# Kernel optimization log

Measured on AMD Instinct MI355X. Metric: run time of the kernel, lower is better.

Reference implementation:

```python
import jax, jax.numpy as jnp
import numpy as np

B, N, D = 2, 2048, 2048
H = 16
HD = D // H          # 128
R = 512              # kv_rank
INT4_MIN, INT4_MAX = -8, 7


def setup_inputs() -> dict:
    key = jax.random.key(0)
    ks = jax.random.split(key, 6)
    sD = 1.0 / np.sqrt(D)
    sR = 1.0 / np.sqrt(R)
    return {
        "x":   jax.random.normal(ks[0], (B, N, D), dtype=jnp.float32),
        "Wq":  jax.random.normal(ks[1], (D, D), dtype=jnp.float32) * sD,
        "bq":  jnp.zeros((D,), dtype=jnp.float32),
        "Wkv": jax.random.normal(ks[2], (D, R), dtype=jnp.float32) * sD,
        "bkv": jnp.zeros((R,), dtype=jnp.float32),
        "Wku": jax.random.normal(ks[3], (R, D), dtype=jnp.float32) * sR,
        "bku": jnp.zeros((D,), dtype=jnp.float32),
        "Wvu": jax.random.normal(ks[4], (R, D), dtype=jnp.float32) * sR,
        "bvu": jnp.zeros((D,), dtype=jnp.float32),
        "Wo":  jax.random.normal(ks[5], (D, D), dtype=jnp.float32) * sD * 0.1,
        "bo":  jnp.zeros((D,), dtype=jnp.float32),
    }


def _int4_quant_dequant(t):
    # per_channel=True, 3D tensor: amax over dims [0,1], keepdim
    amax = jnp.max(jnp.abs(t), axis=(0, 1), keepdims=True)
    amax = jnp.maximum(amax, 1e-5)
    scale = (amax / 7.0).astype(jnp.float32)
    q = jnp.clip(jnp.round(t / scale), INT4_MIN, INT4_MAX).astype(jnp.int8)
    return q.astype(jnp.float32) * scale


def reference(x, Wq, bq, Wkv, bkv, Wku, bku, Wvu, bvu, Wo, bo):
    q = x @ Wq + bq                              # (B,N,D)
    kv_latent = x @ Wkv + bkv                    # (B,N,R)
    kv_latent = _int4_quant_dequant(kv_latent)   # use_cache=True path
    k = kv_latent @ Wku + bku                    # (B,N,D)
    v = kv_latent @ Wvu + bvu                    # (B,N,D)

    q4 = q.reshape(B, N, H, HD)
    k4 = k.reshape(B, N, H, HD)
    v4 = v.reshape(B, N, H, HD)

    attn = jnp.einsum("bqhd,bkhd->bhqk", q4, k4) * (HD ** -0.5)
    attn = jax.nn.softmax(attn.astype(jnp.float32), axis=-1).astype(x.dtype)
    out = jnp.einsum("bhqk,bkhd->bqhd", attn, v4).reshape(B, N, D)
    return out @ Wo + bo
```

## Files before the change

### kernel.cpp

```cpp
#include <hip/hip_runtime.h>
#include <stdint.h>

typedef __attribute__((ext_vector_type(8))) _Float16 half8;
typedef __attribute__((ext_vector_type(4))) _Float16 half4;
typedef __attribute__((ext_vector_type(2))) __fp16 fp16x2;
typedef __attribute__((ext_vector_type(4))) float f32x4;

#define AS1 __attribute__((address_space(1)))
#define AS3 __attribute__((address_space(3)))

__device__ inline void gload_lds16(const void* g, void* l) {
  __builtin_amdgcn_global_load_lds((const AS1 void*)g, (AS3 void*)l, 16, 0, 0);
}
__device__ inline f32x4 mfma16h(half8 a, half8 b, f32x4 c) {
  return __builtin_amdgcn_mfma_f32_16x16x32_f16(a, b, c, 0, 0, 0);
}

__global__ __launch_bounds__(256) void cvt_split(const float4* __restrict__ in,
                                                 half4* __restrict__ xh,
                                                 half4* __restrict__ xl, int nq) {
  int i = blockIdx.x * 256 + threadIdx.x;
  if (i >= nq) return;
  float4 v = in[i];
  float vv[4] = {v.x, v.y, v.z, v.w};
  half4 h, lo;
#pragma unroll
  for (int j = 0; j < 4; ++j) {
    _Float16 hh = (_Float16)vv[j];
    h[j] = hh;
    lo[j] = (_Float16)((vv[j] - (float)hh) * 4096.0f);
  }
  xh[i] = h;
  xl[i] = lo;
}

__global__ __launch_bounds__(256) void transpose_f16(const float* __restrict__ in,
                                                     const float* __restrict__ in2,
                                                     _Float16* __restrict__ outh,
                                                     _Float16* __restrict__ outl,
                                                     const float* __restrict__ rowamax,
                                                     int R, int C) {
  __shared__ float t[32][33];
  if (blockIdx.z) { in = in2; outh += (size_t)R * C; }
  const int tx = threadIdx.x, ty = threadIdx.y;
  const int r0 = blockIdx.y * 32, c0 = blockIdx.x * 32;
#pragma unroll
  for (int k = 0; k < 4; ++k) {
    const int r = r0 + ty + k * 8;
    float s = 1.0f;
    if (rowamax) s = fmaxf(rowamax[r], 1e-5f) / 7.0f;
    t[ty + k * 8][tx] = in[(size_t)r * C + c0 + tx] * s;
  }
  __syncthreads();
#pragma unroll
  for (int k = 0; k < 4; ++k) {
    const int c = c0 + ty + k * 8;
    float v = t[tx][ty + k * 8];
    _Float16 h = (_Float16)v;
    outh[(size_t)c * R + r0 + tx] = h;
    if (outl) outl[(size_t)c * R + r0 + tx] = (_Float16)((v - (float)h) * 4096.0f);
  }
}

__global__ __launch_bounds__(256) void gemm_kv16(const _Float16* __restrict__ Ah,
                                                 const _Float16* __restrict__ Al,
                                                 const _Float16* __restrict__ Bh,
                                                 const _Float16* __restrict__ Bl,
                                                 const float* __restrict__ bias,
                                                 float* __restrict__ C,
                                                 float* __restrict__ amax,
                                                 int M, int N, int K) {
  __shared__ _Float16 sAh[64 * 64], sAl[64 * 64];
  __shared__ _Float16 sBh[64 * 64], sBl[64 * 64];
  const int tid = threadIdx.x;
  const int w = tid >> 6, l = tid & 63, g = l >> 4, c = l & 15;
  const int wr = w >> 1, wc = w & 1;
  int wgid = blockIdx.x + blockIdx.y * gridDim.x;
  const int nwg = gridDim.x * gridDim.y;
  wgid = (wgid & 7) * (nwg >> 3) + (wgid >> 3);
  const int tm0 = (wgid / gridDim.x) * 64, n0 = (wgid % gridDim.x) * 64;

  f32x4 acc[2][2], acc2[2][2];
#pragma unroll
  for (int i = 0; i < 2; ++i)
#pragma unroll
    for (int j = 0; j < 2; ++j) {
      acc[i][j] = f32x4{0.f, 0.f, 0.f, 0.f};
      acc2[i][j] = f32x4{0.f, 0.f, 0.f, 0.f};
    }

  for (int k0 = 0; k0 < K; k0 += 64) {
#pragma unroll
    for (int cc = 0; cc < 2; ++cc) {
      const int off = w * 2048 + cc * 1024 + l * 16;
      const int row = off >> 7, colb = off & 127;
      const char* gA = (const char*)Ah + ((size_t)(tm0 + row) * K + k0) * 2 + colb;
      const char* gL = (const char*)Al + ((size_t)(tm0 + row) * K + k0) * 2 + colb;
      gload_lds16(gA, (char*)sAh + w * 2048 + cc * 1024);
      gload_lds16(gL, (char*)sAl + w * 2048 + cc * 1024);
    }
#pragma unroll
    for (int cc = 0; cc < 2; ++cc) {
      const int off = w * 2048 + cc * 1024 + l * 16;
      const int row = off >> 7, colb = off & 127;
      const char* gB = (const char*)Bh + ((size_t)(n0 + row) * K + k0) * 2 + colb;
      const char* gL = (const char*)Bl + ((size_t)(n0 + row) * K + k0) * 2 + colb;
      gload_lds16(gB, (char*)sBh + w * 2048 + cc * 1024);
      gload_lds16(gL, (char*)sBl + w * 2048 + cc * 1024);
    }
    __syncthreads();
#pragma unroll
    for (int ks = 0; ks < 2; ++ks) {
      half8 ah[2], al[2], bh[2], bl[2];
#pragma unroll
      for (int i = 0; i < 2; ++i) {
        ah[i] = *(const half8*)&sAh[(wr * 32 + i * 16 + c) * 64 + ks * 32 + g * 8];
        al[i] = *(const half8*)&sAl[(wr * 32 + i * 16 + c) * 64 + ks * 32 + g * 8];
      }
#pragma unroll
      for (int j = 0; j < 2; ++j) {
        bh[j] = *(const half8*)&sBh[(wc * 32 + j * 16 + c) * 64 + ks * 32 + g * 8];
        bl[j] = *(const half8*)&sBl[(wc * 32 + j * 16 + c) * 64 + ks * 32 + g * 8];
      }
#pragma unroll
      for (int i = 0; i < 2; ++i)
#pragma unroll
        for (int j = 0; j < 2; ++j) {
          acc[i][j] = mfma16h(ah[i], bh[j], acc[i][j]);
          acc2[i][j] = mfma16h(al[i], bh[j], acc2[i][j]);
          acc2[i][j] = mfma16h(ah[i], bl[j], acc2[i][j]);
        }
    }
    __syncthreads();
  }

  float cm[2] = {0.f, 0.f};
#pragma unroll
  for (int i = 0; i < 2; ++i) {
    const int row0 = tm0 + wr * 32 + i * 16 + g * 4;
#pragma unroll
    for (int j = 0; j < 2; ++j) {
      const int col = n0 + wc * 32 + j * 16 + c;
      const float bv = bias[col];
#pragma unroll
      for (int r = 0; r < 4; ++r) {
        float v = acc[i][j][r] + acc2[i][j][r] * 2.44140625e-4f + bv;
        C[(size_t)(row0 + r) * N + col] = v;
        cm[j] = fmaxf(cm[j], fabsf(v));
      }
    }
  }
#pragma unroll
  for (int j = 0; j < 2; ++j) {
    float m = cm[j];
    m = fmaxf(m, __shfl_xor(m, 16, 64));
    m = fmaxf(m, __shfl_xor(m, 32, 64));
    if (g == 0) atomicMax((int*)amax + (n0 + wc * 32 + j * 16 + c), __float_as_int(m));
  }
}

__global__ __launch_bounds__(256) void quant_kernel(const float4* __restrict__ kv,
                                                    const float* __restrict__ amax,
                                                    half4* __restrict__ kvq, int nq) {
  int i = blockIdx.x * 256 + threadIdx.x;
  if (i >= nq) return;
  float4 v = kv[i];
  int r0 = (i * 4) & 511;
  half4 o;
#pragma unroll
  for (int j = 0; j < 4; ++j) {
    float s = fmaxf(amax[r0 + j], 1e-5f) / 7.0f;
    float val = (j == 0) ? v.x : (j == 1) ? v.y : (j == 2) ? v.z : v.w;
    float q = rintf(val / s);
    q = fminf(7.f, fmaxf(-8.f, q));
    o[j] = (_Float16)q;
  }
  kvq[i] = o;
}

template <int MODE>
__global__ __launch_bounds__(256) void gemm_bt(const _Float16* __restrict__ A,
                                               const _Float16* __restrict__ BT,
                                               void* __restrict__ Cout,
                                               void* __restrict__ Cout2,
                                               const float* __restrict__ bias,
                                               const float* __restrict__ bias2,
                                               float cscale,
                                               int M, int N, int K) {
  __shared__ _Float16 As[128 * 64];
  __shared__ _Float16 Bs[128 * 64];
  const int tid = threadIdx.x;
  const int w = tid >> 6, l = tid & 63, g = l >> 4, c = l & 15;
  const int wr = w >> 1, wc = w & 1;
  int wgid = blockIdx.x + blockIdx.y * gridDim.x;
  const int nwg = gridDim.x * gridDim.y;
  wgid = (wgid & 7) * (nwg >> 3) + (wgid >> 3);
  const int tm0 = (wgid / gridDim.x) * 128, tn0 = (wgid % gridDim.x) * 128;

  f32x4 acc[4][4];
#pragma unroll
  for (int i = 0; i < 4; ++i)
#pragma unroll
    for (int j = 0; j < 4; ++j) acc[i][j] = f32x4{0.f, 0.f, 0.f, 0.f};

  for (int k0 = 0; k0 < K; k0 += 64) {
#pragma unroll
    for (int cc = 0; cc < 4; ++cc) {
      const int off = w * 4096 + cc * 1024 + l * 16;
      const int row = off >> 7, colb = off & 127;
      const char* gA = (const char*)A + ((size_t)(tm0 + row) * K + k0) * 2 + colb;
      const char* gB = (const char*)BT + ((size_t)(tn0 + row) * K + k0) * 2 + colb;
      gload_lds16(gA, (char*)As + w * 4096 + cc * 1024);
      gload_lds16(gB, (char*)Bs + w * 4096 + cc * 1024);
    }
    __syncthreads();
#pragma unroll
    for (int ks = 0; ks < 2; ++ks) {
      half8 a[4], b[4];
#pragma unroll
      for (int i = 0; i < 4; ++i)
        a[i] = *(const half8*)&As[(wr * 64 + i * 16 + c) * 64 + ks * 32 + g * 8];
#pragma unroll
      for (int j = 0; j < 4; ++j)
        b[j] = *(const half8*)&Bs[(wc * 64 + j * 16 + c) * 64 + ks * 32 + g * 8];
#pragma unroll
      for (int i = 0; i < 4; ++i)
#pragma unroll
        for (int j = 0; j < 4; ++j) acc[i][j] = mfma16h(a[i], b[j], acc[i][j]);
    }
    __syncthreads();
  }

#pragma unroll
  for (int i = 0; i < 4; ++i) {
    const int row0 = tm0 + wr * 64 + i * 16 + g * 4;
#pragma unroll
    for (int j = 0; j < 4; ++j) {
      const int col = tn0 + wc * 64 + j * 16 + c;
      if constexpr (MODE == 0) {
        const float bv = bias[col];
#pragma unroll
        for (int r = 0; r < 4; ++r)
          ((_Float16*)Cout)[(size_t)(row0 + r) * N + col] =
              (_Float16)((acc[i][j][r] + bv) * cscale);
      } else if constexpr (MODE == 4) {
        const int bI = row0 >> 11;
        const int colk = col & 2047;
        const int hI = colk >> 7, dI = colk & 127;
        if (col < 2048) {
          const float bv = bias[colk];
#pragma unroll
          for (int r = 0; r < 4; ++r) {
            const int n = (row0 + r) & 2047;
            ((_Float16*)Cout)[(size_t)((bI * 16 + hI) * 32 + (n >> 6)) * 8192 +
                              (n & 63) * 128 + dI] = (_Float16)(acc[i][j][r] + bv);
          }
        } else {
          const float bv = bias2[colk];
          half4 pk;
#pragma unroll
          for (int r = 0; r < 4; ++r) pk[r] = (_Float16)(acc[i][j][r] + bv);
          const int nI = row0 & 2047;
          *(half4*)((_Float16*)Cout2 +
                    (size_t)((bI * 16 + hI) * 32 + (nI >> 6)) * 8192 + dI * 64 + (nI & 63)) = pk;
        }
      } else {
        const float bv = bias[col];
#pragma unroll
        for (int r = 0; r < 4; ++r)
          ((float*)Cout)[(size_t)(row0 + r) * N + col] = acc[i][j][r] + bv;
      }
    }
  }
}

__global__ __launch_bounds__(256, 2) void flash_attn(const _Float16* __restrict__ Q,
                                                     const _Float16* __restrict__ KB,
                                                     const _Float16* __restrict__ VB,
                                                     _Float16* __restrict__ O) {
  __shared__ _Float16 Ks[2][8192];
  __shared__ _Float16 Vs[2][8192];
  __shared__ _Float16 Ps[4][2048];
  const int tid = threadIdx.x, w = tid >> 6, l = tid & 63, g = l >> 4, c = l & 15;
  const int wgid = blockIdx.x + blockIdx.y * 16;
  const int xcd = wgid & 7, idx = wgid >> 3;
  const int bh = xcd * 4 + (idx >> 4), qblk = idx & 15;
  const int b = bh >> 4, h = bh & 15;
  const size_t rowQ0 = (size_t)b * 2048 + qblk * 128 + w * 32;
  const _Float16* kvK = KB + (size_t)bh * 262144;
  const _Float16* kvV = VB + (size_t)bh * 262144;
  const int sw = (c & 7) << 4;

  auto stageK = [&](int t, int buf) {
#pragma unroll
    for (int i = 0; i < 4; ++i) {
      const int o = i * 4096 + w * 1024 + l * 16;
      const int row = o >> 8;
      const int src = (o & ~255) | ((o & 255) ^ ((row & 7) << 4));
      gload_lds16((const char*)(kvK + t * 8192) + src,
                  (char*)&Ks[buf][0] + i * 4096 + w * 1024);
    }
  };
  auto stageV = [&](int t, int buf) {
#pragma unroll
    for (int i = 0; i < 4; ++i) {
      const int o = i * 4096 + w * 1024 + l * 16;
      const int row = o >> 7;
      const int src = (o & ~127) | ((o & 127) ^ ((row & 7) << 4));
      gload_lds16((const char*)(kvV + t * 8192) + src,
                  (char*)&Vs[buf][0] + i * 4096 + w * 1024);
    }
  };

  stageK(0, 0);
  stageV(0, 0);
  half8 bq[2][4];
#pragma unroll
  for (int m = 0; m < 2; ++m)
#pragma unroll
    for (int ks = 0; ks < 4; ++ks)
      bq[m][ks] = *(const half8*)&Q[(rowQ0 + m * 16 + c) * 2048 + h * 128 + ks * 32 + g * 8];

  f32x4 accO[2][8];
#pragma unroll
  for (int m = 0; m < 2; ++m)
#pragma unroll
    for (int n = 0; n < 8; ++n) accO[m][n] = f32x4{0.f, 0.f, 0.f, 0.f};
  float lsum[2] = {0.f, 0.f};

  __syncthreads();

  for (int t = 0; t < 32; ++t) {
    const int cur = t & 1;
    if (t < 31) { stageK(t + 1, cur ^ 1); stageV(t + 1, cur ^ 1); }
    f32x4 accS[2][4];
#pragma unroll
    for (int m = 0; m < 2; ++m)
#pragma unroll
      for (int n = 0; n < 4; ++n) accS[m][n] = f32x4{0.f, 0.f, 0.f, 0.f};
    __builtin_amdgcn_s_setprio(1);
#pragma unroll
    for (int ks = 0; ks < 4; ++ks) {
      half8 ak[4];
#pragma unroll
      for (int n = 0; n < 4; ++n) {
        const int row = n * 16 + c;
        ak[n] = *(const half8*)((const char*)&Ks[cur][0] + row * 256 +
                                ((ks * 64 + g * 16) ^ sw));
      }
#pragma unroll
      for (int m = 0; m < 2; ++m)
#pragma unroll
        for (int n = 0; n < 4; ++n) accS[m][n] = mfma16h(ak[n], bq[m][ks], accS[m][n]);
    }
    __builtin_amdgcn_s_setprio(0);
#pragma unroll
    for (int m = 0; m < 2; ++m)
#pragma unroll
      for (int n = 0; n < 4; ++n) {
        const float p0 = exp2f(accS[m][n][0]);
        const float p1 = exp2f(accS[m][n][1]);
        const float p2 = exp2f(accS[m][n][2]);
        const float p3 = exp2f(accS[m][n][3]);
        lsum[m] += (p0 + p1) + (p2 + p3);
        fp16x2 lo = __builtin_amdgcn_cvt_pkrtz(p0, p1);
        fp16x2 hi = __builtin_amdgcn_cvt_pkrtz(p2, p3);
        uint2 u;
        u.x = __builtin_bit_cast(unsigned, lo);
        u.y = __builtin_bit_cast(unsigned, hi);
        *(uint2*)((char*)&Ps[w][0] + (m * 16 + c) * 128 +
                  ((n * 32 + g * 8) ^ sw)) = u;
      }
    __builtin_amdgcn_s_setprio(1);
#pragma unroll
    for (int ks = 0; ks < 2; ++ks) {
      half8 bp[2];
#pragma unroll
      for (int m = 0; m < 2; ++m)
        bp[m] = *(const half8*)((const char*)&Ps[w][0] + (m * 16 + c) * 128 +
                                ((ks * 64 + g * 16) ^ sw));
#pragma unroll
      for (int n = 0; n < 8; ++n) {
        half8 av = *(const half8*)((const char*)&Vs[cur][0] + (n * 16 + c) * 128 +
                                   ((ks * 64 + g * 16) ^ sw));
#pragma unroll
        for (int m = 0; m < 2; ++m) accO[m][n] = mfma16h(av, bp[m], accO[m][n]);
      }
    }
    __builtin_amdgcn_s_setprio(0);
    __syncthreads();
  }

#pragma unroll
  for (int m = 0; m < 2; ++m) {
    float ps = lsum[m];
    ps += __shfl_xor(ps, 16, 64);
    ps += __shfl_xor(ps, 32, 64);
    const float inv = 1.f / ps;
    const size_t qrow = rowQ0 + m * 16 + c;
#pragma unroll
    for (int n = 0; n < 8; ++n) {
      half4 pk;
#pragma unroll
      for (int r = 0; r < 4; ++r) pk[r] = (_Float16)(accO[m][n][r] * inv);
      *(half4*)&O[qrow * 2048 + h * 128 + n * 16 + g * 4] = pk;
    }
  }
}

#define SCALE_QK 0.08838834764831845f
#define LOG2E    1.4426950408889634f

extern "C" void kernel_launch(void* const* d_in, const int* in_sizes, int n_in,
                              void* d_out, int out_size, void* d_ws, size_t ws_size,
                              hipStream_t stream) {
  const float* x   = (const float*)d_in[0];
  const float* Wq  = (const float*)d_in[1];
  const float* bq  = (const float*)d_in[2];
  const float* Wkv = (const float*)d_in[3];
  const float* bkv = (const float*)d_in[4];
  const float* Wku = (const float*)d_in[5];
  const float* bku = (const float*)d_in[6];
  const float* Wvu = (const float*)d_in[7];
  const float* bvu = (const float*)d_in[8];
  const float* Wo  = (const float*)d_in[9];
  const float* bo  = (const float*)d_in[10];
  float* out = (float*)d_out;

  char* ws = (char*)d_ws;
  const size_t MB = 1ull << 20;
  _Float16* xh   = (_Float16*)(ws + 0 * MB);
  _Float16* attn = (_Float16*)(ws + 0 * MB);
  _Float16* xl   = (_Float16*)(ws + 16 * MB);
  _Float16* qb   = (_Float16*)(ws + 16 * MB);
  _Float16* kb   = (_Float16*)(ws + 32 * MB);
  _Float16* vT   = (_Float16*)(ws + 48 * MB);
  _Float16* WqT  = (_Float16*)(ws + 64 * MB);
  _Float16* WoT  = (_Float16*)(ws + 72 * MB);
  float* kv      = (float*)(ws + 80 * MB);
  _Float16* kvq  = (_Float16*)(ws + 88 * MB);
  _Float16* WkvTh = (_Float16*)(ws + 92 * MB);
  _Float16* WkvTl = (_Float16*)(ws + 94 * MB);
  _Float16* WkuT = (_Float16*)(ws + 96 * MB);
  _Float16* WvuT = (_Float16*)(ws + 98 * MB);
  float* amax    = (float*)(ws + 100 * MB);

  hipMemsetAsync(amax, 0, 512 * sizeof(float), stream);

  cvt_split<<<8192, 256, 0, stream>>>((const float4*)x, (half4*)xh, (half4*)xl, 2097152);
  transpose_f16<<<dim3(64, 64, 2), dim3(32, 8), 0, stream>>>(Wq, Wo, WqT, nullptr, nullptr, 2048, 2048);
  transpose_f16<<<dim3(16, 64), dim3(32, 8), 0, stream>>>(Wkv, nullptr, WkvTh, WkvTl, nullptr, 2048, 512);
  gemm_kv16<<<dim3(8, 64), 256, 0, stream>>>(xh, xl, WkvTh, WkvTl, bkv, kv, amax, 4096, 512, 2048);
  quant_kernel<<<2048, 256, 0, stream>>>((const float4*)kv, amax, (half4*)kvq, 524288);
  transpose_f16<<<dim3(64, 16, 2), dim3(32, 8), 0, stream>>>(Wku, Wvu, WkuT, nullptr, amax, 512, 2048);
  gemm_bt<0><<<dim3(16, 32), 256, 0, stream>>>(xh, WqT, qb, nullptr, bq, nullptr,
                                               SCALE_QK * LOG2E, 4096, 2048, 2048);
  gemm_bt<4><<<dim3(32, 32), 256, 0, stream>>>(kvq, WkuT, kb, vT, bku, bvu, 1.0f,
                                               4096, 4096, 512);
  flash_attn<<<dim3(16, 32), 256, 0, stream>>>(qb, kb, vT, attn);
  gemm_bt<2><<<dim3(16, 32), 256, 0, stream>>>(attn, WoT, out, nullptr, bo, nullptr, 1.0f,
                                               4096, 2048, 2048);

  (void)in_sizes; (void)n_in; (void)out_size; (void)ws_size;
}
```

Before: 319.2 us.

## Split flash attention KV tile across two wave groups with LDS reduction

Doubles the attention block to 512 threads: each group of four waves handles half of every 64-key tile, with K/V staging spread over all eight waves. Partial outputs and row sums from the second group are reduced through shared memory before normalisation and store. The goal is more waves in flight per CU to hide softmax and LDS latency. The cost is an extra reduction step, more LDS traffic at the end, and fewer MFMAs per wave per tile. The softmax has no running max, so splitting keys across groups stays correct.

```diff
diff --git a/kernel.cpp b/kernel.cpp
--- a/kernel.cpp
+++ b/kernel.cpp
@@ -274,41 +274,43 @@
   }
 }
 
-__global__ __launch_bounds__(256, 2) void flash_attn(const _Float16* __restrict__ Q,
+__global__ __launch_bounds__(512, 2) void flash_attn(const _Float16* __restrict__ Q,
                                                      const _Float16* __restrict__ KB,
                                                      const _Float16* __restrict__ VB,
                                                      _Float16* __restrict__ O) {
   __shared__ _Float16 Ks[2][8192];
   __shared__ _Float16 Vs[2][8192];
-  __shared__ _Float16 Ps[4][2048];
+  __shared__ _Float16 Ps[8][1024];
   const int tid = threadIdx.x, w = tid >> 6, l = tid & 63, g = l >> 4, c = l & 15;
+  const int hk = w >> 2, wq = w & 3;
   const int wgid = blockIdx.x + blockIdx.y * 16;
   const int xcd = wgid & 7, idx = wgid >> 3;
   const int bh = xcd * 4 + (idx >> 4), qblk = idx & 15;
   const int b = bh >> 4, h = bh & 15;
-  const size_t rowQ0 = (size_t)b * 2048 + qblk * 128 + w * 32;
+  const size_t rowQ0 = (size_t)b * 2048 + qblk * 128 + wq * 32;
   const _Float16* kvK = KB + (size_t)bh * 262144;
   const _Float16* kvV = VB + (size_t)bh * 262144;
   const int sw = (c & 7) << 4;
+  const int swp = (c & 3) << 4;
 
   auto stageK = [&](int t, int buf) {
 #pragma unroll
-    for (int i = 0; i < 4; ++i) {
-      const int o = i * 4096 + w * 1024 + l * 16;
+    for (int i = 0; i < 2; ++i) {
+      const int o = i * 8192 + tid * 16;
       const int row = o >> 8;
       const int src = (o & ~255) | ((o & 255) ^ ((row & 7) << 4));
       gload_lds16((const char*)(kvK + t * 8192) + src,
-                  (char*)&Ks[buf][0] + i * 4096 + w * 1024);
+                  (char*)&Ks[buf][0] + i * 8192 + w * 1024);
     }
   };
   auto stageV = [&](int t, int buf) {
 #pragma unroll
-    for (int i = 0; i < 4; ++i) {
-      const int o = i * 4096 + w * 1024 + l * 16;
+    for (int i = 0; i < 2; ++i) {
+      const int o = i * 8192 + tid * 16;
       const int row = o >> 7;
       const int src = (o & ~127) | ((o & 127) ^ ((row & 7) << 4));
       gload_lds16((const char*)(kvV + t * 8192) + src,
-                  (char*)&Vs[buf][0] + i * 4096 + w * 1024);
+                  (char*)&Vs[buf][0] + i * 8192 + w * 1024);
     }
   };
 
@@ -333,31 +335,31 @@
   for (int t = 0; t < 32; ++t) {
     const int cur = t & 1;
     if (t < 31) { stageK(t + 1, cur ^ 1); stageV(t + 1, cur ^ 1); }
-    f32x4 accS[2][4];
+    f32x4 accS[2][2];
 #pragma unroll
     for (int m = 0; m < 2; ++m)
 #pragma unroll
-      for (int n = 0; n < 4; ++n) accS[m][n] = f32x4{0.f, 0.f, 0.f, 0.f};
+      for (int n = 0; n < 2; ++n) accS[m][n] = f32x4{0.f, 0.f, 0.f, 0.f};
     __builtin_amdgcn_s_setprio(1);
 #pragma unroll
     for (int ks = 0; ks < 4; ++ks) {
-      half8 ak[4];
-#pragma unroll
-      for (int n = 0; n < 4; ++n) {
-        const int row = n * 16 + c;
+      half8 ak[2];
+#pragma unroll
+      for (int n = 0; n < 2; ++n) {
+        const int row = hk * 32 + n * 16 + c;
         ak[n] = *(const half8*)((const char*)&Ks[cur][0] + row * 256 +
                                 ((ks * 64 + g * 16) ^ sw));
       }
 #pragma unroll
       for (int m = 0; m < 2; ++m)
 #pragma unroll
-        for (int n = 0; n < 4; ++n) accS[m][n] = mfma16h(ak[n], bq[m][ks], accS[m][n]);
+        for (int n = 0; n < 2; ++n) accS[m][n] = mfma16h(ak[n], bq[m][ks], accS[m][n]);
     }
     __builtin_amdgcn_s_setprio(0);
 #pragma unroll
     for (int m = 0; m < 2; ++m)
 #pragma unroll
-      for (int n = 0; n < 4; ++n) {
+      for (int n = 0; n < 2; ++n) {
         const float p0 = exp2f(accS[m][n][0]);
         const float p1 = exp2f(accS[m][n][1]);
         const float p2 = exp2f(accS[m][n][2]);
@@ -368,42 +370,65 @@
         uint2 u;
         u.x = __builtin_bit_cast(unsigned, lo);
         u.y = __builtin_bit_cast(unsigned, hi);
-        *(uint2*)((char*)&Ps[w][0] + (m * 16 + c) * 128 +
-                  ((n * 32 + g * 8) ^ sw)) = u;
+        *(uint2*)((char*)&Ps[w][0] + (m * 16 + c) * 64 +
+                  ((n * 32 + g * 8) ^ swp)) = u;
       }
     __builtin_amdgcn_s_setprio(1);
-#pragma unroll
-    for (int ks = 0; ks < 2; ++ks) {
-      half8 bp[2];
-#pragma unroll
-      for (int m = 0; m < 2; ++m)
-        bp[m] = *(const half8*)((const char*)&Ps[w][0] + (m * 16 + c) * 128 +
-                                ((ks * 64 + g * 16) ^ sw));
-#pragma unroll
-      for (int n = 0; n < 8; ++n) {
-        half8 av = *(const half8*)((const char*)&Vs[cur][0] + (n * 16 + c) * 128 +
-                                   ((ks * 64 + g * 16) ^ sw));
-#pragma unroll
-        for (int m = 0; m < 2; ++m) accO[m][n] = mfma16h(av, bp[m], accO[m][n]);
-      }
+    half8 bp[2];
+#pragma unroll
+    for (int m = 0; m < 2; ++m)
+      bp[m] = *(const half8*)((const char*)&Ps[w][0] + (m * 16 + c) * 64 +
+                              ((g * 16) ^ swp));
+#pragma unroll
+    for (int n = 0; n < 8; ++n) {
+      half8 av = *(const half8*)((const char*)&Vs[cur][0] + (n * 16 + c) * 128 +
+                                 ((hk * 64 + g * 16) ^ sw));
+      accO[0][n] = mfma16h(av, bp[0], accO[0][n]);
+      accO[1][n] = mfma16h(av, bp[1], accO[1][n]);
     }
     __builtin_amdgcn_s_setprio(0);
     __syncthreads();
   }
 
-#pragma unroll
-  for (int m = 0; m < 2; ++m) {
-    float ps = lsum[m];
-    ps += __shfl_xor(ps, 16, 64);
-    ps += __shfl_xor(ps, 32, 64);
-    const float inv = 1.f / ps;
-    const size_t qrow = rowQ0 + m * 16 + c;
-#pragma unroll
-    for (int n = 0; n < 8; ++n) {
-      half4 pk;
-#pragma unroll
-      for (int r = 0; r < 4; ++r) pk[r] = (_Float16)(accO[m][n][r] * inv);
-      *(half4*)&O[qrow * 2048 + h * 128 + n * 16 + g * 4] = pk;
+  float* redO0 = (float*)&Ks[0][0];
+  float* redO1 = (float*)&Vs[0][0];
+  float* redL  = (float*)&Ps[0][0];
+  if (hk == 1) {
+#pragma unroll
+    for (int n = 0; n < 8; ++n)
+#pragma unroll
+      for (int r = 0; r < 4; ++r) {
+        redO0[(wq * 64 + l) * 32 + n * 4 + r] = accO[0][n][r];
+        redO1[(wq * 64 + l) * 32 + n * 4 + r] = accO[1][n][r];
+      }
+    redL[(wq * 64 + l) * 2 + 0] = lsum[0];
+    redL[(wq * 64 + l) * 2 + 1] = lsum[1];
+  }
+  __syncthreads();
+  if (hk == 0) {
+#pragma unroll
+    for (int n = 0; n < 8; ++n)
+#pragma unroll
+      for (int r = 0; r < 4; ++r) {
+        accO[0][n][r] += redO0[(wq * 64 + l) * 32 + n * 4 + r];
+        accO[1][n][r] += redO1[(wq * 64 + l) * 32 + n * 4 + r];
+      }
+    lsum[0] += redL[(wq * 64 + l) * 2 + 0];
+    lsum[1] += redL[(wq * 64 + l) * 2 + 1];
+#pragma unroll
+    for (int m = 0; m < 2; ++m) {
+      float ps = lsum[m];
+      ps += __shfl_xor(ps, 16, 64);
+      ps += __shfl_xor(ps, 32, 64);
+      const float inv = 1.f / ps;
+      const size_t qrow = rowQ0 + m * 16 + c;
+#pragma unroll
+      for (int n = 0; n < 8; ++n) {
+        half4 pk;
+#pragma unroll
+        for (int r = 0; r < 4; ++r) pk[r] = (_Float16)(accO[m][n][r] * inv);
+        *(half4*)&O[qrow * 2048 + h * 128 + n * 16 + g * 4] = pk;
+      }
     }
   }
 }
@@ -457,7 +482,7 @@
                                                SCALE_QK * LOG2E, 4096, 2048, 2048);
   gemm_bt<4><<<dim3(32, 32), 256, 0, stream>>>(kvq, WkuT, kb, vT, bku, bvu, 1.0f,
                                                4096, 4096, 512);
-  flash_attn<<<dim3(16, 32), 256, 0, stream>>>(qb, kb, vT, attn);
+  flash_attn<<<dim3(16, 32), 512, 0, stream>>>(qb, kb, vT, attn);
   gemm_bt<2><<<dim3(16, 32), 256, 0, stream>>>(attn, WoT, out, nullptr, bo, nullptr, 1.0f,
                                                4096, 2048, 2048);
 
```

After: 348.5 us. +9.2%, slower.
